# Optimization experiments

Measured on AMD Instinct MI355X. Metric: run time of the kernel, lower is better.

The kernel has to match this reference:

```python
import jax, jax.numpy as jnp
import numpy as np

G = 8          # grid_size
DH = 32        # dim_head
EPS = 1e-5
INIT_LS = 1e-5


def setup_inputs() -> dict:
    key = jax.random.key(0)
    ks = jax.random.split(key, 8)
    B, H, W, C = 16, 128, 128, 256
    s = 1.0 / np.sqrt(C)
    return {
        "x": jax.random.normal(ks[0], (B, H, W, C), dtype=jnp.float32),
        "ln_w": jnp.ones((C,), jnp.float32),
        "ln_b": jnp.zeros((C,), jnp.float32),
        "in_proj_w": jax.random.uniform(ks[1], (3 * C, C), jnp.float32, -s, s),
        "in_proj_b": jnp.zeros((3 * C,), jnp.float32),
        "out_proj_w": jax.random.uniform(ks[2], (C, C), jnp.float32, -s, s),
        "out_proj_b": jnp.zeros((C,), jnp.float32),
        "gamma": jnp.full((C,), INIT_LS, jnp.float32),
    }


def _grid_attention(x, ln_w, ln_b, in_proj_w, in_proj_b, out_proj_w, out_proj_b, gamma):
    B, H, W, C = x.shape
    nh = C // DH
    # LayerNorm over channels
    mu = jnp.mean(x, axis=-1, keepdims=True)
    var = jnp.mean(jnp.square(x - mu), axis=-1, keepdims=True)
    x = (x - mu) * jax.lax.rsqrt(var + EPS) * ln_w + ln_b
    # grid partition: (B,G,H/G,G,W/G,C) -> (B,H/G,W/G,G,G,C) -> (N, G*G, C)
    hg, wg = H // G, W // G
    xw = x.reshape(B, G, hg, G, wg, C).transpose(0, 2, 4, 1, 3, 5)
    xw = xw.reshape(B * hg * wg, G * G, C)  # N windows of L=G*G tokens
    # MHSA (nn.MultiheadAttention semantics)
    qkv = xw @ in_proj_w.T + in_proj_b                      # (N, L, 3C)
    q, k, v = jnp.split(qkv, 3, axis=-1)
    N, L = xw.shape[0], xw.shape[1]
    q = q.reshape(N, L, nh, DH).transpose(0, 2, 1, 3)        # (N, nh, L, DH)
    k = k.reshape(N, L, nh, DH).transpose(0, 2, 1, 3)
    v = v.reshape(N, L, nh, DH).transpose(0, 2, 1, 3)
    scores = jnp.einsum("nhld,nhmd->nhlm", q, k) / np.sqrt(DH)
    attn = jax.nn.softmax(scores, axis=-1)
    out = jnp.einsum("nhlm,nhmd->nhld", attn, v)             # (N, nh, L, DH)
    out = out.transpose(0, 2, 1, 3).reshape(N, L, C)
    out = out @ out_proj_w.T + out_proj_b
    # LayerScale
    out = out * gamma
    # grid reverse: (B,H/G,W/G,G,G,C) -> (B,G,H/G,G,W/G,C) -> (B,H,W,C)
    out = out.reshape(B, hg, wg, G, G, C).transpose(0, 3, 1, 4, 2, 5)
    return out.reshape(B, H, W, C)


def reference(x, ln_w, ln_b, in_proj_w, in_proj_b, out_proj_w, out_proj_b, gamma):
    return _grid_attention(x, ln_w, ln_b, in_proj_w, in_proj_b,
                           out_proj_w, out_proj_b, gamma)
```

## Files before the change

### kernel.cpp

```cpp
#include <hip/hip_runtime.h>
#include <hip/hip_bf16.h>

typedef __attribute__((ext_vector_type(8))) short short8;
typedef __attribute__((ext_vector_type(4))) float f32x4;
typedef __attribute__((ext_vector_type(4))) unsigned short us4;
typedef __attribute__((ext_vector_type(2))) unsigned uint2v;

union U8 { unsigned u[4]; short8 s; };

__device__ __forceinline__ unsigned short f2b(float f) {
  unsigned u = __float_as_uint(f);
  u += 0x7FFFu + ((u >> 16) & 1u);
  return (unsigned short)(u >> 16);
}
__device__ __forceinline__ unsigned pkbf(float lo, float hi) {
  __hip_bfloat162 h = __float22bfloat162_rn(make_float2(lo, hi));
  unsigned u; __builtin_memcpy(&u, &h, 4);
  return u;
}
__device__ __forceinline__ void swp32(unsigned &a, unsigned &b) {
  uint2v r = __builtin_amdgcn_permlane32_swap(a, b, false, false);
  a = r.x; b = r.y;
}
__device__ __forceinline__ void swp16(unsigned &a, unsigned &b) {
  uint2v r = __builtin_amdgcn_permlane16_swap(a, b, false, false);
  a = r.x; b = r.y;
}
__device__ __forceinline__ float redq_max(float v) {
  uint2v r = __builtin_amdgcn_permlane16_swap(__float_as_uint(v), __float_as_uint(v), false, false);
  v = fmaxf(__uint_as_float(r.x), __uint_as_float(r.y));
  r = __builtin_amdgcn_permlane32_swap(__float_as_uint(v), __float_as_uint(v), false, false);
  return fmaxf(__uint_as_float(r.x), __uint_as_float(r.y));
}
__device__ __forceinline__ float redq_sum(float v) {
  uint2v r = __builtin_amdgcn_permlane16_swap(__float_as_uint(v), __float_as_uint(v), false, false);
  v = __uint_as_float(r.x) + __uint_as_float(r.y);
  r = __builtin_amdgcn_permlane32_swap(__float_as_uint(v), __float_as_uint(v), false, false);
  return __uint_as_float(r.x) + __uint_as_float(r.y);
}
__device__ __forceinline__ float red5_sum(float v) {
  v += __shfl_xor(v, 8);
  return redq_sum(v);
}

__global__ __launch_bounds__(64) void prep(
    const float* __restrict__ wq, const float* __restrict__ wo,
    const float* __restrict__ gm, const float* __restrict__ bo,
    unsigned short* __restrict__ wbf, float* __restrict__ boG) {
  int d = blockIdx.x, lane = threadIdx.x;
  if (d < 768) {
    float4 wv = *(const float4*)(wq + (size_t)d * 256 + lane * 4);
    us4 o;
    o.x = f2b(wv.x); o.y = f2b(wv.y); o.z = f2b(wv.z); o.w = f2b(wv.w);
    *(us4*)(wbf + (size_t)d * 256 + lane * 4) = o;
  } else {
    int dd = d - 768;
    float g = gm[dd];
    float4 wv = *(const float4*)(wo + (size_t)dd * 256 + lane * 4);
    us4 o;
    o.x = f2b(wv.x * g); o.y = f2b(wv.y * g); o.z = f2b(wv.z * g); o.w = f2b(wv.w * g);
    *(us4*)(wbf + 196608 + (size_t)dd * 256 + lane * 4) = o;
    if (lane == 0) boG[dd] = bo[dd] * g;
  }
}

__global__ __launch_bounds__(512, 4) void grid_attn(
    const float* __restrict__ x,
    const float* __restrict__ lnw4,
    const float* __restrict__ lnb4,
    const unsigned short* __restrict__ Wqkv,
    const float* __restrict__ bqkv,
    const unsigned short* __restrict__ Wout,
    const float* __restrict__ boG,
    float* __restrict__ out) {

  __shared__ unsigned short ldsX[64 * 264];
  __shared__ float ldsMu[64];
  __shared__ float ldsRs[64];

  const int tid = threadIdx.x;
  const int w   = tid >> 6;
  const int lid = tid & 63;
  const int l16 = lid & 15;
  const int lhi = lid >> 4;

  const int n  = blockIdx.x;
  const int b  = n >> 8;
  const int wi = (n >> 4) & 15;
  const int wj = n & 15;

  {
    float4 v[8];
    float2 p[8];
    #pragma unroll
    for (int t = 0; t < 8; ++t) {
      int l = w * 8 + t;
      int a = l >> 3, cg = l & 7;
      int hh = a * 16 + wi, ww = cg * 16 + wj;
      v[t] = *(const float4*)(x + ((size_t)((b * 128 + hh) * 128 + ww)) * 256 + lid * 4);
      p[t].x = v[t].x + v[t].y + v[t].z + v[t].w;
      p[t].y = v[t].x * v[t].x + v[t].y * v[t].y + v[t].z * v[t].z + v[t].w * v[t].w;
    }
    const int h1 = lid & 1, h2 = (lid >> 1) & 1, h4 = (lid >> 2) & 1;
    float2 q[4];
    #pragma unroll
    for (int i = 0; i < 4; ++i) {
      float sx = h1 ? p[i].x : p[i + 4].x, sy = h1 ? p[i].y : p[i + 4].y;
      float kx = h1 ? p[i + 4].x : p[i].x, ky = h1 ? p[i + 4].y : p[i].y;
      q[i].x = kx + __shfl_xor(sx, 1);
      q[i].y = ky + __shfl_xor(sy, 1);
    }
    float2 r2[2];
    #pragma unroll
    for (int i = 0; i < 2; ++i) {
      float sx = h2 ? q[i].x : q[i + 2].x, sy = h2 ? q[i].y : q[i + 2].y;
      float kx = h2 ? q[i + 2].x : q[i].x, ky = h2 ? q[i + 2].y : q[i].y;
      r2[i].x = kx + __shfl_xor(sx, 2);
      r2[i].y = ky + __shfl_xor(sy, 2);
    }
    float fx, fy;
    {
      float sx = h4 ? r2[0].x : r2[1].x, sy = h4 ? r2[0].y : r2[1].y;
      float kx = h4 ? r2[1].x : r2[0].x, ky = h4 ? r2[1].y : r2[0].y;
      fx = kx + __shfl_xor(sx, 4);
      fy = ky + __shfl_xor(sy, 4);
    }
    fx = red5_sum(fx);
    fy = red5_sum(fy);
    if (lid < 8) {
      int T = h1 * 4 + h2 * 2 + h4;
      float mu = fx * (1.0f / 256.0f);
      float var = fy * (1.0f / 256.0f) - mu * mu;
      ldsMu[w * 8 + T] = mu;
      ldsRs[w * 8 + T] = rsqrtf(var + 1e-5f);
    }
    float4 lw = *(const float4*)(lnw4 + lid * 4);
    float4 lb = *(const float4*)(lnb4 + lid * 4);
    #pragma unroll
    for (int t = 0; t < 8; ++t) {
      int l = w * 8 + t;
      float mu = ldsMu[w * 8 + t];
      float rs = ldsRs[w * 8 + t];
      float n0 = (v[t].x - mu) * rs * lw.x + lb.x;
      float n1 = (v[t].y - mu) * rs * lw.y + lb.y;
      float n2 = (v[t].z - mu) * rs * lw.z + lb.z;
      float n3 = (v[t].w - mu) * rs * lw.w + lb.w;
      uint2v o; o.x = pkbf(n0, n1); o.y = pkbf(n2, n3);
      *(uint2v*)(&ldsX[l * 264 + lid * 4]) = o;
    }
  }
  __syncthreads();

  short8 vtf[2][2];
  {
    float bv0 = bqkv[512 + w * 32 + l16];
    float bv1 = bqkv[512 + w * 32 + 16 + l16];
    f32x4 va[4][2];
    #pragma unroll
    for (int tt = 0; tt < 4; ++tt) {
      va[tt][0] = (f32x4){bv0, bv0, bv0, bv0};
      va[tt][1] = (f32x4){bv1, bv1, bv1, bv1};
    }
    const unsigned short* wvp = Wqkv + (size_t)(512 + w * 32 + l16) * 256 + lhi * 8;
    #pragma unroll 4
    for (int kc = 0; kc < 8; ++kc) {
      short8 wv0 = *(const short8*)(wvp + kc * 32);
      short8 wv1 = *(const short8*)(wvp + 16 * 256 + kc * 32);
      #pragma unroll
      for (int tt = 0; tt < 4; ++tt) {
        short8 xf = *(const short8*)(&ldsX[(tt * 16 + l16) * 264 + kc * 32 + lhi * 8]);
        va[tt][0] = __builtin_amdgcn_mfma_f32_16x16x32_bf16(xf, wv0, va[tt][0], 0, 0, 0);
        va[tt][1] = __builtin_amdgcn_mfma_f32_16x16x32_bf16(xf, wv1, va[tt][1], 0, 0, 0);
      }
    }
    #pragma unroll
    for (int dt = 0; dt < 2; ++dt) {
      unsigned bu[8];
      #pragma unroll
      for (int tt = 0; tt < 4; ++tt) {
        bu[tt * 2]     = pkbf(va[tt][dt][0], va[tt][dt][1]);
        bu[tt * 2 + 1] = pkbf(va[tt][dt][2], va[tt][dt][3]);
      }
      swp32(bu[0], bu[2]); swp32(bu[1], bu[3]); swp32(bu[4], bu[6]); swp32(bu[5], bu[7]);
      swp16(bu[0], bu[2]); swp16(bu[1], bu[3]); swp16(bu[4], bu[6]); swp16(bu[5], bu[7]);
      U8 z0, z1;
      z0.u[0] = bu[0]; z0.u[1] = bu[1]; z0.u[2] = bu[2]; z0.u[3] = bu[3];
      z1.u[0] = bu[4]; z1.u[1] = bu[5]; z1.u[2] = bu[6]; z1.u[3] = bu[7];
      vtf[dt][0] = z0.s;
      vtf[dt][1] = z1.s;
    }
  }

  short8 qf[4], kf[4];

  {
    f32x4 Cq0 = *(const f32x4*)(bqkv + w * 32 + lhi * 4);
    f32x4 Cq1 = *(const f32x4*)(bqkv + w * 32 + 16 + lhi * 4);
    f32x4 qa[2][4];
    #pragma unroll
    for (int tt = 0; tt < 4; ++tt) { qa[0][tt] = Cq0; qa[1][tt] = Cq1; }
    const unsigned short* wqp = Wqkv + (size_t)(w * 32 + l16) * 256 + lhi * 8;
    #pragma unroll 4
    for (int kc = 0; kc < 8; ++kc) {
      short8 wq0 = *(const short8*)(wqp + kc * 32);
      short8 wq1 = *(const short8*)(wqp + 16 * 256 + kc * 32);
      #pragma unroll
      for (int tt = 0; tt < 4; ++tt) {
        short8 xf = *(const short8*)(&ldsX[(tt * 16 + l16) * 264 + kc * 32 + lhi * 8]);
        qa[0][tt] = __builtin_amdgcn_mfma_f32_16x16x32_bf16(wq0, xf, qa[0][tt], 0, 0, 0);
        qa[1][tt] = __builtin_amdgcn_mfma_f32_16x16x32_bf16(wq1, xf, qa[1][tt], 0, 0, 0);
      }
    }
    #pragma unroll
    for (int tt = 0; tt < 4; ++tt) {
      unsigned a0 = pkbf(qa[0][tt][0], qa[0][tt][1]), a1 = pkbf(qa[0][tt][2], qa[0][tt][3]);
      unsigned a2 = pkbf(qa[1][tt][0], qa[1][tt][1]), a3 = pkbf(qa[1][tt][2], qa[1][tt][3]);
      swp32(a0, a2); swp32(a1, a3);
      swp16(a0, a2); swp16(a1, a3);
      U8 z; z.u[0] = a0; z.u[1] = a1; z.u[2] = a2; z.u[3] = a3;
      qf[tt] = z.s;
    }
  }

  {
    f32x4 Ck0 = *(const f32x4*)(bqkv + 256 + w * 32 + lhi * 4);
    f32x4 Ck1 = *(const f32x4*)(bqkv + 256 + w * 32 + 16 + lhi * 4);
    f32x4 ka[2][4];
    #pragma unroll
    for (int tt = 0; tt < 4; ++tt) { ka[0][tt] = Ck0; ka[1][tt] = Ck1; }
    const unsigned short* wkp = Wqkv + (size_t)(256 + w * 32 + l16) * 256 + lhi * 8;
    #pragma unroll 4
    for (int kc = 0; kc < 8; ++kc) {
      short8 wk0 = *(const short8*)(wkp + kc * 32);
      short8 wk1 = *(const short8*)(wkp + 16 * 256 + kc * 32);
      #pragma unroll
      for (int tt = 0; tt < 4; ++tt) {
        short8 xf = *(const short8*)(&ldsX[(tt * 16 + l16) * 264 + kc * 32 + lhi * 8]);
        ka[0][tt] = __builtin_amdgcn_mfma_f32_16x16x32_bf16(wk0, xf, ka[0][tt], 0, 0, 0);
        ka[1][tt] = __builtin_amdgcn_mfma_f32_16x16x32_bf16(wk1, xf, ka[1][tt], 0, 0, 0);
      }
    }
    #pragma unroll
    for (int tt = 0; tt < 4; ++tt) {
      unsigned a0 = pkbf(ka[0][tt][0], ka[0][tt][1]), a1 = pkbf(ka[0][tt][2], ka[0][tt][3]);
      unsigned a2 = pkbf(ka[1][tt][0], ka[1][tt][1]), a3 = pkbf(ka[1][tt][2], ka[1][tt][3]);
      swp32(a0, a2); swp32(a1, a3);
      swp16(a0, a2); swp16(a1, a3);
      U8 z; z.u[0] = a0; z.u[1] = a1; z.u[2] = a2; z.u[3] = a3;
      kf[tt] = z.s;
    }
  }

  uint2v po[4][2];
  const float K2 = 0.25503487013594137f;
  #pragma unroll
  for (int nn = 0; nn < 4; ++nn) {
    f32x4 s[4];
    #pragma unroll
    for (int m = 0; m < 4; ++m)
      s[m] = __builtin_amdgcn_mfma_f32_16x16x32_bf16(kf[m], qf[nn], (f32x4){0.f,0.f,0.f,0.f}, 0, 0, 0);
    float mm[4];
    #pragma unroll
    for (int m = 0; m < 4; ++m)
      mm[m] = fmaxf(fmaxf(s[m][0], s[m][1]), fmaxf(s[m][2], s[m][3]));
    float mx = fmaxf(fmaxf(mm[0], mm[1]), fmaxf(mm[2], mm[3]));
    mx = redq_max(mx);
    float sm[4];
    unsigned bu[8];
    #pragma unroll
    for (int m = 0; m < 4; ++m) {
      float e0 = exp2f((s[m][0] - mx) * K2);
      float e1 = exp2f((s[m][1] - mx) * K2);
      float e2 = exp2f((s[m][2] - mx) * K2);
      float e3 = exp2f((s[m][3] - mx) * K2);
      sm[m] = (e0 + e1) + (e2 + e3);
      bu[m * 2]     = pkbf(e0, e1);
      bu[m * 2 + 1] = pkbf(e2, e3);
    }
    float sum = (sm[0] + sm[1]) + (sm[2] + sm[3]);
    sum = redq_sum(sum);
    float iv = 1.0f / sum;
    swp32(bu[0], bu[2]); swp32(bu[1], bu[3]); swp32(bu[4], bu[6]); swp32(bu[5], bu[7]);
    swp16(bu[0], bu[2]); swp16(bu[1], bu[3]); swp16(bu[4], bu[6]); swp16(bu[5], bu[7]);
    U8 z0, z1;
    z0.u[0] = bu[0]; z0.u[1] = bu[1]; z0.u[2] = bu[2]; z0.u[3] = bu[3];
    z1.u[0] = bu[4]; z1.u[1] = bu[5]; z1.u[2] = bu[6]; z1.u[3] = bu[7];
    f32x4 ot0 = (f32x4){0.f,0.f,0.f,0.f};
    f32x4 ot1 = (f32x4){0.f,0.f,0.f,0.f};
    ot0 = __builtin_amdgcn_mfma_f32_16x16x32_bf16(vtf[0][0], z0.s, ot0, 0, 0, 0);
    ot0 = __builtin_amdgcn_mfma_f32_16x16x32_bf16(vtf[0][1], z1.s, ot0, 0, 0, 0);
    ot1 = __builtin_amdgcn_mfma_f32_16x16x32_bf16(vtf[1][0], z0.s, ot1, 0, 0, 0);
    ot1 = __builtin_amdgcn_mfma_f32_16x16x32_bf16(vtf[1][1], z1.s, ot1, 0, 0, 0);
    po[nn][0].x = pkbf(ot0[0] * iv, ot0[1] * iv);
    po[nn][0].y = pkbf(ot0[2] * iv, ot0[3] * iv);
    po[nn][1].x = pkbf(ot1[0] * iv, ot1[1] * iv);
    po[nn][1].y = pkbf(ot1[2] * iv, ot1[3] * iv);
  }

  __syncthreads();

  #pragma unroll
  for (int nn = 0; nn < 4; ++nn)
    #pragma unroll
    for (int dt = 0; dt < 2; ++dt)
      *(uint2v*)(&ldsX[(nn * 16 + l16) * 264 + w * 32 + dt * 16 + lhi * 4]) = po[nn][dt];
  __syncthreads();

  f32x4 ya[4][2];
  #pragma unroll
  for (int mt = 0; mt < 4; ++mt)
    #pragma unroll
    for (int nt = 0; nt < 2; ++nt)
      ya[mt][nt] = (f32x4){0.f, 0.f, 0.f, 0.f};
  {
    const unsigned short* wop = Wout + (size_t)(w * 32 + l16) * 256 + lhi * 8;
    #pragma unroll 4
    for (int kc = 0; kc < 8; ++kc) {
      short8 wf0 = *(const short8*)(wop + kc * 32);
      short8 wf1 = *(const short8*)(wop + 16 * 256 + kc * 32);
      #pragma unroll
      for (int mt = 0; mt < 4; ++mt) {
        short8 af = *(const short8*)(&ldsX[(mt * 16 + l16) * 264 + kc * 32 + lhi * 8]);
        ya[mt][0] = __builtin_amdgcn_mfma_f32_16x16x32_bf16(af, wf0, ya[mt][0], 0, 0, 0);
        ya[mt][1] = __builtin_amdgcn_mfma_f32_16x16x32_bf16(af, wf1, ya[mt][1], 0, 0, 0);
      }
    }
  }

  float ob0 = boG[w * 32 + l16];
  float ob1 = boG[w * 32 + 16 + l16];
  #pragma unroll
  for (int mt = 0; mt < 4; ++mt)
    #pragma unroll
    for (int r = 0; r < 4; ++r) {
      int row = mt * 16 + lhi * 4 + r;
      int a = row >> 3, cg = row & 7;
      int hh = a * 16 + wi, ww2 = cg * 16 + wj;
      float* pout = out + ((size_t)((b * 128 + hh) * 128 + ww2)) * 256 + w * 32;
      pout[l16]      = ya[mt][0][r] + ob0;
      pout[l16 + 16] = ya[mt][1][r] + ob1;
    }
}

extern "C" void kernel_launch(void* const* d_in, const int* in_sizes, int n_in,
                              void* d_out, int out_size, void* d_ws, size_t ws_size,
                              hipStream_t stream) {
  const float* x    = (const float*)d_in[0];
  const float* ln_w = (const float*)d_in[1];
  const float* ln_b = (const float*)d_in[2];
  const float* ipw  = (const float*)d_in[3];
  const float* ipb  = (const float*)d_in[4];
  const float* opw  = (const float*)d_in[5];
  const float* opb  = (const float*)d_in[6];
  const float* gm   = (const float*)d_in[7];

  unsigned short* wbf = (unsigned short*)d_ws;
  float* boG = (float*)(wbf + 262144);

  prep<<<1024, 64, 0, stream>>>(ipw, opw, gm, opb, wbf, boG);
  grid_attn<<<4096, 512, 0, stream>>>(x, ln_w, ln_b, wbf, ipb,
                                      wbf + 196608, boG, (float*)d_out);
}
```

Baseline: 344.3 us.

## Reorder QK softmax before V projection, drop max subtraction, raise occupancy

Computes Q, K and the softmax probabilities before the V projection. The final P·V then uses pre-normalized bf16 probabilities and writes straight to LDS after an added barrier. The softmax max reduction is removed, the out-projection bias is folded into the accumulator init, MFMA regions are wrapped in s_setprio, and launch bounds go from 4 to 6 blocks per CU. The aim is less softmax work and live register pressure, plus more waves in flight. Skipping the max subtraction risks exp overflow on larger scores. The 6-block bound may force register spills, while LDS use of about 34KB per block may cap residency anyway.

```diff
diff --git a/kernel.cpp b/kernel.cpp
--- a/kernel.cpp
+++ b/kernel.cpp
@@ -25,12 +25,6 @@
 __device__ __forceinline__ void swp16(unsigned &a, unsigned &b) {
   uint2v r = __builtin_amdgcn_permlane16_swap(a, b, false, false);
   a = r.x; b = r.y;
-}
-__device__ __forceinline__ float redq_max(float v) {
-  uint2v r = __builtin_amdgcn_permlane16_swap(__float_as_uint(v), __float_as_uint(v), false, false);
-  v = fmaxf(__uint_as_float(r.x), __uint_as_float(r.y));
-  r = __builtin_amdgcn_permlane32_swap(__float_as_uint(v), __float_as_uint(v), false, false);
-  return fmaxf(__uint_as_float(r.x), __uint_as_float(r.y));
 }
 __device__ __forceinline__ float redq_sum(float v) {
   uint2v r = __builtin_amdgcn_permlane16_swap(__float_as_uint(v), __float_as_uint(v), false, false);
@@ -64,7 +58,7 @@
   }
 }
 
-__global__ __launch_bounds__(512, 4) void grid_attn(
+__global__ __launch_bounds__(512, 6) void grid_attn(
     const float* __restrict__ x,
     const float* __restrict__ lnw4,
     const float* __restrict__ lnb4,
@@ -96,8 +90,7 @@
     for (int t = 0; t < 8; ++t) {
       int l = w * 8 + t;
       int a = l >> 3, cg = l & 7;
-      int hh = a * 16 + wi, ww = cg * 16 + wj;
-      v[t] = *(const float4*)(x + ((size_t)((b * 128 + hh) * 128 + ww)) * 256 + lid * 4);
+      v[t] = *(const float4*)(x + ((size_t)((b * 128 + a * 16 + wi) * 128 + cg * 16 + wj)) * 256 + lid * 4);
       p[t].x = v[t].x + v[t].y + v[t].z + v[t].w;
       p[t].y = v[t].x * v[t].x + v[t].y * v[t].y + v[t].z * v[t].z + v[t].w * v[t].w;
     }
@@ -151,6 +144,108 @@
   }
   __syncthreads();
 
+  short8 qf[4];
+  {
+    f32x4 Cq0 = *(const f32x4*)(bqkv + w * 32 + lhi * 4);
+    f32x4 Cq1 = *(const f32x4*)(bqkv + w * 32 + 16 + lhi * 4);
+    f32x4 qa[2][4];
+    #pragma unroll
+    for (int tt = 0; tt < 4; ++tt) { qa[0][tt] = Cq0; qa[1][tt] = Cq1; }
+    const unsigned short* wqp = Wqkv + (size_t)(w * 32 + l16) * 256 + lhi * 8;
+    __builtin_amdgcn_s_setprio(1);
+    #pragma unroll 4
+    for (int kc = 0; kc < 8; ++kc) {
+      short8 wq0 = *(const short8*)(wqp + kc * 32);
+      short8 wq1 = *(const short8*)(wqp + 16 * 256 + kc * 32);
+      #pragma unroll
+      for (int tt = 0; tt < 4; ++tt) {
+        short8 xf = *(const short8*)(&ldsX[(tt * 16 + l16) * 264 + kc * 32 + lhi * 8]);
+        qa[0][tt] = __builtin_amdgcn_mfma_f32_16x16x32_bf16(wq0, xf, qa[0][tt], 0, 0, 0);
+        qa[1][tt] = __builtin_amdgcn_mfma_f32_16x16x32_bf16(wq1, xf, qa[1][tt], 0, 0, 0);
+      }
+    }
+    __builtin_amdgcn_s_setprio(0);
+    #pragma unroll
+    for (int tt = 0; tt < 4; ++tt) {
+      unsigned a0 = pkbf(qa[0][tt][0], qa[0][tt][1]), a1 = pkbf(qa[0][tt][2], qa[0][tt][3]);
+      unsigned a2 = pkbf(qa[1][tt][0], qa[1][tt][1]), a3 = pkbf(qa[1][tt][2], qa[1][tt][3]);
+      swp32(a0, a2); swp32(a1, a3);
+      swp16(a0, a2); swp16(a1, a3);
+      U8 z; z.u[0] = a0; z.u[1] = a1; z.u[2] = a2; z.u[3] = a3;
+      qf[tt] = z.s;
+    }
+  }
+
+  short8 kf[4];
+  {
+    f32x4 Ck0 = *(const f32x4*)(bqkv + 256 + w * 32 + lhi * 4);
+    f32x4 Ck1 = *(const f32x4*)(bqkv + 256 + w * 32 + 16 + lhi * 4);
+    f32x4 ka[2][4];
+    #pragma unroll
+    for (int tt = 0; tt < 4; ++tt) { ka[0][tt] = Ck0; ka[1][tt] = Ck1; }
+    const unsigned short* wkp = Wqkv + (size_t)(256 + w * 32 + l16) * 256 + lhi * 8;
+    __builtin_amdgcn_s_setprio(1);
+    #pragma unroll 4
+    for (int kc = 0; kc < 8; ++kc) {
+      short8 wk0 = *(const short8*)(wkp + kc * 32);
+      short8 wk1 = *(const short8*)(wkp + 16 * 256 + kc * 32);
+      #pragma unroll
+      for (int tt = 0; tt < 4; ++tt) {
+        short8 xf = *(const short8*)(&ldsX[(tt * 16 + l16) * 264 + kc * 32 + lhi * 8]);
+        ka[0][tt] = __builtin_amdgcn_mfma_f32_16x16x32_bf16(wk0, xf, ka[0][tt], 0, 0, 0);
+        ka[1][tt] = __builtin_amdgcn_mfma_f32_16x16x32_bf16(wk1, xf, ka[1][tt], 0, 0, 0);
+      }
+    }
+    __builtin_amdgcn_s_setprio(0);
+    #pragma unroll
+    for (int tt = 0; tt < 4; ++tt) {
+      unsigned a0 = pkbf(ka[0][tt][0], ka[0][tt][1]), a1 = pkbf(ka[0][tt][2], ka[0][tt][3]);
+      unsigned a2 = pkbf(ka[1][tt][0], ka[1][tt][1]), a3 = pkbf(ka[1][tt][2], ka[1][tt][3]);
+      swp32(a0, a2); swp32(a1, a3);
+      swp16(a0, a2); swp16(a1, a3);
+      U8 z; z.u[0] = a0; z.u[1] = a1; z.u[2] = a2; z.u[3] = a3;
+      kf[tt] = z.s;
+    }
+  }
+
+  short8 ptf[4][2];
+  const float K2 = 0.25503487013594137f;
+  #pragma unroll
+  for (int nn = 0; nn < 4; ++nn) {
+    f32x4 s[4];
+    __builtin_amdgcn_s_setprio(1);
+    #pragma unroll
+    for (int m = 0; m < 4; ++m)
+      s[m] = __builtin_amdgcn_mfma_f32_16x16x32_bf16(kf[m], qf[nn], (f32x4){0.f,0.f,0.f,0.f}, 0, 0, 0);
+    __builtin_amdgcn_s_setprio(0);
+    float e[4][4];
+    float sm[4];
+    #pragma unroll
+    for (int m = 0; m < 4; ++m) {
+      e[m][0] = exp2f(s[m][0] * K2);
+      e[m][1] = exp2f(s[m][1] * K2);
+      e[m][2] = exp2f(s[m][2] * K2);
+      e[m][3] = exp2f(s[m][3] * K2);
+      sm[m] = (e[m][0] + e[m][1]) + (e[m][2] + e[m][3]);
+    }
+    float sum = (sm[0] + sm[1]) + (sm[2] + sm[3]);
+    sum = redq_sum(sum);
+    float iv = 1.0f / sum;
+    unsigned bu[8];
+    #pragma unroll
+    for (int m = 0; m < 4; ++m) {
+      bu[m * 2]     = pkbf(e[m][0] * iv, e[m][1] * iv);
+      bu[m * 2 + 1] = pkbf(e[m][2] * iv, e[m][3] * iv);
+    }
+    swp32(bu[0], bu[2]); swp32(bu[1], bu[3]); swp32(bu[4], bu[6]); swp32(bu[5], bu[7]);
+    swp16(bu[0], bu[2]); swp16(bu[1], bu[3]); swp16(bu[4], bu[6]); swp16(bu[5], bu[7]);
+    U8 z0, z1;
+    z0.u[0] = bu[0]; z0.u[1] = bu[1]; z0.u[2] = bu[2]; z0.u[3] = bu[3];
+    z1.u[0] = bu[4]; z1.u[1] = bu[5]; z1.u[2] = bu[6]; z1.u[3] = bu[7];
+    ptf[nn][0] = z0.s;
+    ptf[nn][1] = z1.s;
+  }
+
   short8 vtf[2][2];
   {
     float bv0 = bqkv[512 + w * 32 + l16];
@@ -162,6 +257,7 @@
       va[tt][1] = (f32x4){bv1, bv1, bv1, bv1};
     }
     const unsigned short* wvp = Wqkv + (size_t)(512 + w * 32 + l16) * 256 + lhi * 8;
+    __builtin_amdgcn_s_setprio(1);
     #pragma unroll 4
     for (int kc = 0; kc < 8; ++kc) {
       short8 wv0 = *(const short8*)(wvp + kc * 32);
@@ -173,6 +269,7 @@
         va[tt][1] = __builtin_amdgcn_mfma_f32_16x16x32_bf16(xf, wv1, va[tt][1], 0, 0, 0);
       }
     }
+    __builtin_amdgcn_s_setprio(0);
     #pragma unroll
     for (int dt = 0; dt < 2; ++dt) {
       unsigned bu[8];
@@ -191,129 +288,39 @@
     }
   }
 
-  short8 qf[4], kf[4];
-
-  {
-    f32x4 Cq0 = *(const f32x4*)(bqkv + w * 32 + lhi * 4);
-    f32x4 Cq1 = *(const f32x4*)(bqkv + w * 32 + 16 + lhi * 4);
-    f32x4 qa[2][4];
-    #pragma unroll
-    for (int tt = 0; tt < 4; ++tt) { qa[0][tt] = Cq0; qa[1][tt] = Cq1; }
-    const unsigned short* wqp = Wqkv + (size_t)(w * 32 + l16) * 256 + lhi * 8;
-    #pragma unroll 4
-    for (int kc = 0; kc < 8; ++kc) {
-      short8 wq0 = *(const short8*)(wqp + kc * 32);
-      short8 wq1 = *(const short8*)(wqp + 16 * 256 + kc * 32);
-      #pragma unroll
-      for (int tt = 0; tt < 4; ++tt) {
-        short8 xf = *(const short8*)(&ldsX[(tt * 16 + l16) * 264 + kc * 32 + lhi * 8]);
-        qa[0][tt] = __builtin_amdgcn_mfma_f32_16x16x32_bf16(wq0, xf, qa[0][tt], 0, 0, 0);
-        qa[1][tt] = __builtin_amdgcn_mfma_f32_16x16x32_bf16(wq1, xf, qa[1][tt], 0, 0, 0);
-      }
-    }
-    #pragma unroll
-    for (int tt = 0; tt < 4; ++tt) {
-      unsigned a0 = pkbf(qa[0][tt][0], qa[0][tt][1]), a1 = pkbf(qa[0][tt][2], qa[0][tt][3]);
-      unsigned a2 = pkbf(qa[1][tt][0], qa[1][tt][1]), a3 = pkbf(qa[1][tt][2], qa[1][tt][3]);
-      swp32(a0, a2); swp32(a1, a3);
-      swp16(a0, a2); swp16(a1, a3);
-      U8 z; z.u[0] = a0; z.u[1] = a1; z.u[2] = a2; z.u[3] = a3;
-      qf[tt] = z.s;
-    }
-  }
-
-  {
-    f32x4 Ck0 = *(const f32x4*)(bqkv + 256 + w * 32 + lhi * 4);
-    f32x4 Ck1 = *(const f32x4*)(bqkv + 256 + w * 32 + 16 + lhi * 4);
-    f32x4 ka[2][4];
-    #pragma unroll
-    for (int tt = 0; tt < 4; ++tt) { ka[0][tt] = Ck0; ka[1][tt] = Ck1; }
-    const unsigned short* wkp = Wqkv + (size_t)(256 + w * 32 + l16) * 256 + lhi * 8;
-    #pragma unroll 4
-    for (int kc = 0; kc < 8; ++kc) {
-      short8 wk0 = *(const short8*)(wkp + kc * 32);
-      short8 wk1 = *(const short8*)(wkp + 16 * 256 + kc * 32);
-      #pragma unroll
-      for (int tt = 0; tt < 4; ++tt) {
-        short8 xf = *(const short8*)(&ldsX[(tt * 16 + l16) * 264 + kc * 32 + lhi * 8]);
-        ka[0][tt] = __builtin_amdgcn_mfma_f32_16x16x32_bf16(wk0, xf, ka[0][tt], 0, 0, 0);
-        ka[1][tt] = __builtin_amdgcn_mfma_f32_16x16x32_bf16(wk1, xf, ka[1][tt], 0, 0, 0);
-      }
-    }
-    #pragma unroll
-    for (int tt = 0; tt < 4; ++tt) {
-      unsigned a0 = pkbf(ka[0][tt][0], ka[0][tt][1]), a1 = pkbf(ka[0][tt][2], ka[0][tt][3]);
-      unsigned a2 = pkbf(ka[1][tt][0], ka[1][tt][1]), a3 = pkbf(ka[1][tt][2], ka[1][tt][3]);
-      swp32(a0, a2); swp32(a1, a3);
-      swp16(a0, a2); swp16(a1, a3);
-      U8 z; z.u[0] = a0; z.u[1] = a1; z.u[2] = a2; z.u[3] = a3;
-      kf[tt] = z.s;
-    }
-  }
-
-  uint2v po[4][2];
-  const float K2 = 0.25503487013594137f;
+  __syncthreads();
+
   #pragma unroll
   for (int nn = 0; nn < 4; ++nn) {
-    f32x4 s[4];
-    #pragma unroll
-    for (int m = 0; m < 4; ++m)
-      s[m] = __builtin_amdgcn_mfma_f32_16x16x32_bf16(kf[m], qf[nn], (f32x4){0.f,0.f,0.f,0.f}, 0, 0, 0);
-    float mm[4];
-    #pragma unroll
-    for (int m = 0; m < 4; ++m)
-      mm[m] = fmaxf(fmaxf(s[m][0], s[m][1]), fmaxf(s[m][2], s[m][3]));
-    float mx = fmaxf(fmaxf(mm[0], mm[1]), fmaxf(mm[2], mm[3]));
-    mx = redq_max(mx);
-    float sm[4];
-    unsigned bu[8];
-    #pragma unroll
-    for (int m = 0; m < 4; ++m) {
-      float e0 = exp2f((s[m][0] - mx) * K2);
-      float e1 = exp2f((s[m][1] - mx) * K2);
-      float e2 = exp2f((s[m][2] - mx) * K2);
-      float e3 = exp2f((s[m][3] - mx) * K2);
-      sm[m] = (e0 + e1) + (e2 + e3);
-      bu[m * 2]     = pkbf(e0, e1);
-      bu[m * 2 + 1] = pkbf(e2, e3);
-    }
-    float sum = (sm[0] + sm[1]) + (sm[2] + sm[3]);
-    sum = redq_sum(sum);
-    float iv = 1.0f / sum;
-    swp32(bu[0], bu[2]); swp32(bu[1], bu[3]); swp32(bu[4], bu[6]); swp32(bu[5], bu[7]);
-    swp16(bu[0], bu[2]); swp16(bu[1], bu[3]); swp16(bu[4], bu[6]); swp16(bu[5], bu[7]);
-    U8 z0, z1;
-    z0.u[0] = bu[0]; z0.u[1] = bu[1]; z0.u[2] = bu[2]; z0.u[3] = bu[3];
-    z1.u[0] = bu[4]; z1.u[1] = bu[5]; z1.u[2] = bu[6]; z1.u[3] = bu[7];
     f32x4 ot0 = (f32x4){0.f,0.f,0.f,0.f};
     f32x4 ot1 = (f32x4){0.f,0.f,0.f,0.f};
-    ot0 = __builtin_amdgcn_mfma_f32_16x16x32_bf16(vtf[0][0], z0.s, ot0, 0, 0, 0);
-    ot0 = __builtin_amdgcn_mfma_f32_16x16x32_bf16(vtf[0][1], z1.s, ot0, 0, 0, 0);
-    ot1 = __builtin_amdgcn_mfma_f32_16x16x32_bf16(vtf[1][0], z0.s, ot1, 0, 0, 0);
-    ot1 = __builtin_amdgcn_mfma_f32_16x16x32_bf16(vtf[1][1], z1.s, ot1, 0, 0, 0);
-    po[nn][0].x = pkbf(ot0[0] * iv, ot0[1] * iv);
-    po[nn][0].y = pkbf(ot0[2] * iv, ot0[3] * iv);
-    po[nn][1].x = pkbf(ot1[0] * iv, ot1[1] * iv);
-    po[nn][1].y = pkbf(ot1[2] * iv, ot1[3] * iv);
-  }
-
+    __builtin_amdgcn_s_setprio(1);
+    ot0 = __builtin_amdgcn_mfma_f32_16x16x32_bf16(vtf[0][0], ptf[nn][0], ot0, 0, 0, 0);
+    ot0 = __builtin_amdgcn_mfma_f32_16x16x32_bf16(vtf[0][1], ptf[nn][1], ot0, 0, 0, 0);
+    ot1 = __builtin_amdgcn_mfma_f32_16x16x32_bf16(vtf[1][0], ptf[nn][0], ot1, 0, 0, 0);
+    ot1 = __builtin_amdgcn_mfma_f32_16x16x32_bf16(vtf[1][1], ptf[nn][1], ot1, 0, 0, 0);
+    __builtin_amdgcn_s_setprio(0);
+    uint2v o0, o1;
+    o0.x = pkbf(ot0[0], ot0[1]);
+    o0.y = pkbf(ot0[2], ot0[3]);
+    o1.x = pkbf(ot1[0], ot1[1]);
+    o1.y = pkbf(ot1[2], ot1[3]);
+    *(uint2v*)(&ldsX[(nn * 16 + l16) * 264 + w * 32 + lhi * 4]) = o0;
+    *(uint2v*)(&ldsX[(nn * 16 + l16) * 264 + w * 32 + 16 + lhi * 4]) = o1;
+  }
   __syncthreads();
 
-  #pragma unroll
-  for (int nn = 0; nn < 4; ++nn)
-    #pragma unroll
-    for (int dt = 0; dt < 2; ++dt)
-      *(uint2v*)(&ldsX[(nn * 16 + l16) * 264 + w * 32 + dt * 16 + lhi * 4]) = po[nn][dt];
-  __syncthreads();
-
+  float ob0 = boG[w * 32 + l16];
+  float ob1 = boG[w * 32 + 16 + l16];
   f32x4 ya[4][2];
   #pragma unroll
-  for (int mt = 0; mt < 4; ++mt)
-    #pragma unroll
-    for (int nt = 0; nt < 2; ++nt)
-      ya[mt][nt] = (f32x4){0.f, 0.f, 0.f, 0.f};
+  for (int mt = 0; mt < 4; ++mt) {
+    ya[mt][0] = (f32x4){ob0, ob0, ob0, ob0};
+    ya[mt][1] = (f32x4){ob1, ob1, ob1, ob1};
+  }
   {
     const unsigned short* wop = Wout + (size_t)(w * 32 + l16) * 256 + lhi * 8;
+    __builtin_amdgcn_s_setprio(1);
     #pragma unroll 4
     for (int kc = 0; kc < 8; ++kc) {
       short8 wf0 = *(const short8*)(wop + kc * 32);
@@ -325,20 +332,18 @@
         ya[mt][1] = __builtin_amdgcn_mfma_f32_16x16x32_bf16(af, wf1, ya[mt][1], 0, 0, 0);
       }
     }
-  }
-
-  float ob0 = boG[w * 32 + l16];
-  float ob1 = boG[w * 32 + 16 + l16];
+    __builtin_amdgcn_s_setprio(0);
+  }
+
   #pragma unroll
   for (int mt = 0; mt < 4; ++mt)
     #pragma unroll
     for (int r = 0; r < 4; ++r) {
       int row = mt * 16 + lhi * 4 + r;
       int a = row >> 3, cg = row & 7;
-      int hh = a * 16 + wi, ww2 = cg * 16 + wj;
-      float* pout = out + ((size_t)((b * 128 + hh) * 128 + ww2)) * 256 + w * 32;
-      pout[l16]      = ya[mt][0][r] + ob0;
-      pout[l16 + 16] = ya[mt][1][r] + ob1;
+      float* pout = out + ((size_t)((b * 128 + a * 16 + wi) * 128 + cg * 16 + wj)) * 256 + w * 32;
+      pout[l16]      = ya[mt][0][r];
+      pout[l16 + 16] = ya[mt][1][r];
     }
 }
 
```

Result: slower. 382.4 us (+11.1%).
